# Kernel tuning notes

Hardware: AMD Instinct MI355X
Metric: run time of the kernel (lower is better)

Reference implementation:

```python
import jax, jax.numpy as jnp
import numpy as np

EPS = 1e-8
NS = 1e9  # nanoseconds per second


def qmult(a, b):
    aw, ax, ay, az = a[..., 0], a[..., 1], a[..., 2], a[..., 3]
    bw, bx, by, bz = b[..., 0], b[..., 1], b[..., 2], b[..., 3]
    return jnp.stack([
        aw * bw - ax * bx - ay * by - az * bz,
        aw * bx + ax * bw + ay * bz - az * by,
        aw * by - ax * bz + ay * bw + az * bx,
        aw * bz + ax * by - ay * bx + az * bw,
    ], axis=-1)


def qinv(q):
    # unit-quaternion inverse == conjugate
    return q * jnp.array([1.0, -1.0, -1.0, -1.0], dtype=q.dtype)


def qexp(v):
    # log-quaternion (..., 3) -> unit quaternion (..., 4)
    n = jnp.maximum(jnp.linalg.norm(v, axis=-1, keepdims=True), EPS)
    return jnp.concatenate([jnp.cos(n), jnp.sin(n) / n * v], axis=-1)


def qlog(q):
    # unit quaternion (..., 4) -> log-quaternion (..., 3)
    n = jnp.maximum(jnp.linalg.norm(q[..., 1:], axis=-1, keepdims=True), EPS)
    return q[..., 1:] * jnp.arccos(jnp.clip(q[..., :1], -1.0, 1.0)) / n


def rotate_vec(v, q):
    # rotate vector v (..., 3) by quaternion q (..., 4)
    vq = jnp.concatenate([jnp.zeros_like(v[..., :1]), v], axis=-1)
    return qmult(qmult(q, vq), qinv(q))[..., 1:]


def l1(a, b):
    return jnp.mean(jnp.abs(a - b))


def setup_inputs() -> dict:
    key = jax.random.key(0)
    k1, k2, k3 = jax.random.split(key, 3)
    N, T = 2048, 1024
    pred = jax.random.normal(k1, (N, T, 6), dtype=jnp.float32)
    targ = jax.random.normal(k2, (N, T, 6), dtype=jnp.float32)
    imu = jax.random.normal(k3, (N, T, 10), dtype=jnp.float32)
    ts = jnp.broadcast_to(jnp.arange(T, dtype=jnp.float32) * 5e6, (N, T))
    imu = imu.at[..., 9].set(ts)
    z = jnp.zeros((1,), dtype=jnp.float32)
    return {"pred": pred, "targ": targ, "imu": imu,
            "sax": z, "saq": z, "srx": z, "srq": z}


def reference(pred, targ, imu, sax, saq, srx, srq):
    # ---- absolute pose loss ----
    abs_loss = (jnp.exp(-sax) * l1(pred[..., :3], targ[..., :3]) + sax
                + jnp.exp(-saq) * l1(pred[..., 3:], targ[..., 3:]) + saq)

    # ---- simple VOs: consecutive differences (N, T-1, 6) ----
    pred_vos = pred[:, 1:] - pred[:, :-1]
    targ_vos = targ[:, 1:] - targ[:, :-1]

    # ---- true relative poses from targ (calc_vos) ----
    q0 = qexp(targ[:, :-1, 3:])            # (N, T-1, 4)
    q1 = qexp(targ[:, 1:, 3:])
    q0i = qinv(q0)
    targ_imu_q = qlog(qmult(q0i, q1))      # (N, T-1, 3) rotation part of calc_vos

    # ---- IMU integration (vectorized over the original N x T python loop) ----
    ts = imu[..., 9]
    dt = ((ts[:, 1:] - ts[:, :-1]) / NS)[..., None]   # (N, T-1, 1) seconds
    accel = imu[:, :-1, 0:3]
    vel = imu[:, :-1, 3:6]
    ang_vel = imu[:, :-1, 6:9]
    imu_trans = vel * dt + 0.5 * accel * dt * dt       # (N, T-1, 3)

    wnorm = jnp.maximum(jnp.linalg.norm(ang_vel, axis=-1, keepdims=True), EPS)
    theta = wnorm * dt                                  # rotation angle over dt
    dq = jnp.concatenate([jnp.cos(0.5 * theta),
                          (ang_vel / wnorm) * jnp.sin(0.5 * theta)], axis=-1)
    new_q = jax.lax.stop_gradient(qmult(q0, dq))        # numpy round-trip in torch detaches
    imu_ori_shift = qlog(qmult(q0i, new_q))             # (N, T-1, 3)

    # ---- relative (VO) loss ----
    vo_loss = (jnp.exp(-srx) * l1(pred_vos[..., :3], targ_vos[..., :3]) + srx
               + jnp.exp(-srq) * l1(pred_vos[..., 3:], targ_vos[..., 3:]) + srq)

    # ---- IMU loss ----
    imu_loss = (jnp.exp(-srx) * l1(pred_vos[..., :3], imu_trans) + srx
                + jnp.exp(-srq) * l1(targ_imu_q, imu_ori_shift) + srq)

    return abs_loss + vo_loss + imu_loss   # shape (1,)
```

## Files before the change

kernel.cpp:

```cpp
#include <hip/hip_runtime.h>
#include <math.h>

#define NN 2048
#define TT 1024
#define EPSF 1e-8f

#define BLOCK    256
#define GRID     2048
#define NPAIR    (NN * TT / 2)
#define NTHREADS (GRID * BLOCK)
#define PITER    (NPAIR / NTHREADS)
#define PAIRS_PER_N (TT / 2)

struct Quat { float w, x, y, z; };

__device__ inline Quat qmul(const Quat a, const Quat b) {
    Quat r;
    r.w = a.w * b.w - a.x * b.x - a.y * b.y - a.z * b.z;
    r.x = a.w * b.x + a.x * b.w + a.y * b.z - a.z * b.y;
    r.y = a.w * b.y - a.x * b.z + a.y * b.w + a.z * b.x;
    r.z = a.w * b.z + a.x * b.y - a.y * b.x + a.z * b.w;
    return r;
}

__device__ inline Quat qconj(const Quat q) {
    Quat r; r.w = q.w; r.x = -q.x; r.y = -q.y; r.z = -q.z; return r;
}

__device__ inline Quat qexp3(float vx, float vy, float vz) {
    float n = fmaxf(sqrtf(vx * vx + vy * vy + vz * vz), EPSF);
    float s = __sinf(n) / n;
    Quat r;
    r.w = __cosf(n);
    r.x = s * vx; r.y = s * vy; r.z = s * vz;
    return r;
}

__device__ inline void qlog3(const Quat q, float& ox, float& oy, float& oz) {
    float n = fmaxf(sqrtf(q.x * q.x + q.y * q.y + q.z * q.z), EPSF);
    float c = fminf(fmaxf(q.w, -1.0f), 1.0f);
    float s = acosf(c) / n;
    ox = q.x * s; oy = q.y * s; oz = q.z * s;
}

__device__ inline float waveReduceF(float v) {
    #pragma unroll
    for (int o = 32; o > 0; o >>= 1) v += __shfl_down(v, o);
    return v;
}

__device__ inline double waveReduceD(double v) {
    #pragma unroll
    for (int o = 32; o > 0; o >>= 1) v += __shfl_down(v, o);
    return v;
}

__device__ inline void pair_terms(
    const float pa[6], const float pb[6], const float ga[6], const float gb[6],
    const Quat qR, const Quat qN,
    float a0, float a1, float a2, float v0, float v1, float v2,
    float w0, float w1, float w2, float ts0, float ts1,
    float& s2, float& s3, float& s4, float& s5)
{
    float pv0 = pb[0] - pa[0], pv1 = pb[1] - pa[1], pv2 = pb[2] - pa[2];
    float pv3 = pb[3] - pa[3], pv4 = pb[4] - pa[4], pv5 = pb[5] - pa[5];
    float tv0 = gb[0] - ga[0], tv1 = gb[1] - ga[1], tv2 = gb[2] - ga[2];
    float tv3 = gb[3] - ga[3], tv4 = gb[4] - ga[4], tv5 = gb[5] - ga[5];

    s2 += fabsf(pv0 - tv0) + fabsf(pv1 - tv1) + fabsf(pv2 - tv2);
    s3 += fabsf(pv3 - tv3) + fabsf(pv4 - tv4) + fabsf(pv5 - tv5);

    Quat qRi = qconj(qR);
    Quat r01 = qmul(qRi, qN);
    float tq0, tq1, tq2;
    qlog3(r01, tq0, tq1, tq2);

    float dt = (ts1 - ts0) * 1e-9f;
    float hdt2 = 0.5f * dt * dt;
    float it0 = v0 * dt + a0 * hdt2;
    float it1 = v1 * dt + a1 * hdt2;
    float it2 = v2 * dt + a2 * hdt2;
    s4 += fabsf(pv0 - it0) + fabsf(pv1 - it1) + fabsf(pv2 - it2);

    float wn = fmaxf(sqrtf(w0 * w0 + w1 * w1 + w2 * w2), EPSF);
    float half = 0.5f * wn * dt;
    float sd = __sinf(half) / wn;
    Quat dq; dq.w = __cosf(half); dq.x = w0 * sd; dq.y = w1 * sd; dq.z = w2 * sd;
    Quat nq = qmul(qR, dq);
    Quat m  = qmul(qRi, nq);
    float io0, io1, io2;
    qlog3(m, io0, io1, io2);
    s5 += fabsf(tq0 - io0) + fabsf(tq1 - io1) + fabsf(tq2 - io2);
}

__global__ __launch_bounds__(BLOCK) void loss_main(
    const float* __restrict__ pred, const float* __restrict__ targ,
    const float* __restrict__ imu, float* __restrict__ partial)
{
    float s0 = 0.f, s1 = 0.f, s2 = 0.f, s3 = 0.f, s4 = 0.f, s5 = 0.f;
    const int base = blockIdx.x * BLOCK + threadIdx.x;

    #pragma unroll
    for (int k = 0; k < PITER; ++k) {
        const int u = base + k * NTHREADS;
        const int tp = u & (PAIRS_PER_N - 1);

        const float4* p4 = reinterpret_cast<const float4*>(pred) + (size_t)u * 3;
        const float4* g4 = reinterpret_cast<const float4*>(targ) + (size_t)u * 3;
        const float4* i4 = reinterpret_cast<const float4*>(imu)  + (size_t)u * 5;

        float4 P0 = p4[0], P1 = p4[1], P2 = p4[2];
        float4 G0 = g4[0], G1 = g4[1], G2 = g4[2];
        float4 I0 = i4[0], I1 = i4[1], I2 = i4[2], I3 = i4[3], I4 = i4[4];

        float pA[6] = {P0.x, P0.y, P0.z, P0.w, P1.x, P1.y};
        float pB[6] = {P1.z, P1.w, P2.x, P2.y, P2.z, P2.w};
        float gA[6] = {G0.x, G0.y, G0.z, G0.w, G1.x, G1.y};
        float gB[6] = {G1.z, G1.w, G2.x, G2.y, G2.z, G2.w};

        s0 += fabsf(pA[0]-gA[0]) + fabsf(pA[1]-gA[1]) + fabsf(pA[2]-gA[2])
            + fabsf(pB[0]-gB[0]) + fabsf(pB[1]-gB[1]) + fabsf(pB[2]-gB[2]);
        s1 += fabsf(pA[3]-gA[3]) + fabsf(pA[4]-gA[4]) + fabsf(pA[5]-gA[5])
            + fabsf(pB[3]-gB[3]) + fabsf(pB[4]-gB[4]) + fabsf(pB[5]-gB[5]);

        Quat qA = qexp3(gA[3], gA[4], gA[5]);
        Quat qB = qexp3(gB[3], gB[4], gB[5]);

        float tsA = I2.y, tsB = I4.w;

        pair_terms(pA, pB, gA, gB, qA, qB,
                   I0.x, I0.y, I0.z,
                   I0.w, I1.x, I1.y,
                   I1.z, I1.w, I2.x,
                   tsA, tsB, s2, s3, s4, s5);

        if (tp != PAIRS_PER_N - 1) {
            float4 P3 = p4[3];
            float2 PF = reinterpret_cast<const float2*>(pred)[(size_t)u * 6 + 8];
            float4 G3 = g4[3];
            float2 GF = reinterpret_cast<const float2*>(targ)[(size_t)u * 6 + 8];
            float tsC = imu[(size_t)u * 20 + 29];

            float pC[6] = {P3.x, P3.y, P3.z, P3.w, PF.x, PF.y};
            float gC[6] = {G3.x, G3.y, G3.z, G3.w, GF.x, GF.y};

            Quat qC = qexp3(gC[3], gC[4], gC[5]);

            pair_terms(pB, pC, gB, gC, qB, qC,
                       I2.z, I2.w, I3.x,
                       I3.y, I3.z, I3.w,
                       I4.x, I4.y, I4.z,
                       tsB, tsC, s2, s3, s4, s5);
        }
    }

    s0 = waveReduceF(s0); s1 = waveReduceF(s1); s2 = waveReduceF(s2);
    s3 = waveReduceF(s3); s4 = waveReduceF(s4); s5 = waveReduceF(s5);

    __shared__ float red[4][6];
    const int lane = threadIdx.x & 63;
    const int wid  = threadIdx.x >> 6;
    if (lane == 0) {
        red[wid][0] = s0; red[wid][1] = s1; red[wid][2] = s2;
        red[wid][3] = s3; red[wid][4] = s4; red[wid][5] = s5;
    }
    __syncthreads();
    if (threadIdx.x < 6) {
        const int c = threadIdx.x;
        partial[(size_t)blockIdx.x * 6 + c] = red[0][c] + red[1][c] + red[2][c] + red[3][c];
    }
}

__global__ __launch_bounds__(256) void loss_finalize(
    const float* __restrict__ partial,
    const float* __restrict__ sax, const float* __restrict__ saq,
    const float* __restrict__ srx, const float* __restrict__ srq,
    float* __restrict__ out)
{
    double t0 = 0, t1 = 0, t2 = 0, t3 = 0, t4 = 0, t5 = 0;
    for (int r = threadIdx.x; r < GRID; r += 256) {
        const float* p = partial + (size_t)r * 6;
        t0 += p[0]; t1 += p[1]; t2 += p[2];
        t3 += p[3]; t4 += p[4]; t5 += p[5];
    }
    t0 = waveReduceD(t0); t1 = waveReduceD(t1); t2 = waveReduceD(t2);
    t3 = waveReduceD(t3); t4 = waveReduceD(t4); t5 = waveReduceD(t5);

    __shared__ double red[4][6];
    const int lane = threadIdx.x & 63;
    const int wid  = threadIdx.x >> 6;
    if (lane == 0) {
        red[wid][0] = t0; red[wid][1] = t1; red[wid][2] = t2;
        red[wid][3] = t3; red[wid][4] = t4; red[wid][5] = t5;
    }
    __syncthreads();
    if (threadIdx.x == 0) {
        double a0 = 0, a1 = 0, a2 = 0, a3 = 0, a4 = 0, a5 = 0;
        #pragma unroll
        for (int w = 0; w < 4; ++w) {
            a0 += red[w][0]; a1 += red[w][1]; a2 += red[w][2];
            a3 += red[w][3]; a4 += red[w][4]; a5 += red[w][5];
        }
        const double inv_abs = 1.0 / ((double)NN * TT * 3);
        const double inv_vo  = 1.0 / ((double)NN * (TT - 1) * 3);
        float A = (float)(a0 * inv_abs);
        float B = (float)(a1 * inv_abs);
        float C = (float)(a2 * inv_vo);
        float D = (float)(a3 * inv_vo);
        float E = (float)(a4 * inv_vo);
        float F = (float)(a5 * inv_vo);
        float sx = sax[0], sq = saq[0], rx = srx[0], rq = srq[0];
        out[0] = expf(-sx) * A + sx + expf(-sq) * B + sq
               + expf(-rx) * (C + E) + 2.0f * rx
               + expf(-rq) * (D + F) + 2.0f * rq;
    }
}

extern "C" void kernel_launch(void* const* d_in, const int* in_sizes, int n_in,
                              void* d_out, int out_size, void* d_ws, size_t ws_size,
                              hipStream_t stream) {
    const float* pred = (const float*)d_in[0];
    const float* targ = (const float*)d_in[1];
    const float* imu  = (const float*)d_in[2];
    const float* sax  = (const float*)d_in[3];
    const float* saq  = (const float*)d_in[4];
    const float* srx  = (const float*)d_in[5];
    const float* srq  = (const float*)d_in[6];
    float* out = (float*)d_out;
    float* partial = (float*)d_ws;

    loss_main<<<GRID, BLOCK, 0, stream>>>(pred, targ, imu, partial);
    loss_finalize<<<1, 256, 0, stream>>>(partial, sax, saq, srx, srq, out);
}
```

Before: 209.9 us.

## Stage rows in LDS, simplify IMU quaternion log, use fast sqrt/rcp/acos

Each block now handles half of one sequence. It stages pred, targ and imu for that half in shared memory with coalesced float4 loads, so neighbour samples are read from shared memory instead of being reloaded from global memory. The IMU orientation term qlog(conj(q)*q*dq) is replaced by the closed form 0.5*dt*w, which removes two quaternion products, a sin/cos and an acos per pair. acosf, sqrt and division are also swapped for a polynomial acos approximation and hardware sqrt/rcp builtins. These trade accuracy for fewer instructions, and the closed form diverges from the reference when |w|*dt/2 exceeds pi or w is near zero.

```diff
diff --git a/kernel.cpp b/kernel.cpp
--- a/kernel.cpp
+++ b/kernel.cpp
@@ -4,15 +4,23 @@
 #define NN 2048
 #define TT 1024
 #define EPSF 1e-8f
-
-#define BLOCK    256
-#define GRID     2048
-#define NPAIR    (NN * TT / 2)
-#define NTHREADS (GRID * BLOCK)
-#define PITER    (NPAIR / NTHREADS)
-#define PAIRS_PER_N (TT / 2)
+#define BLOCK 256
+#define HALF 512
+#define NBLK (NN * 2)
 
 struct Quat { float w, x, y, z; };
+
+__device__ inline float fsqrt_f(float x) { return __builtin_amdgcn_sqrtf(x); }
+__device__ inline float frcp_f(float x)  { return __builtin_amdgcn_rcpf(x); }
+
+__device__ inline float acos_fast(float x) {
+    float ax = fabsf(x);
+    float p = fmaf(ax, -0.0187293f, 0.0742610f);
+    p = fmaf(ax, p, -0.2121144f);
+    p = fmaf(ax, p, 1.5707288f);
+    float r = fsqrt_f(1.0f - ax) * p;
+    return x >= 0.0f ? r : 3.14159274f - r;
+}
 
 __device__ inline Quat qmul(const Quat a, const Quat b) {
     Quat r;
@@ -28,18 +36,18 @@
 }
 
 __device__ inline Quat qexp3(float vx, float vy, float vz) {
-    float n = fmaxf(sqrtf(vx * vx + vy * vy + vz * vz), EPSF);
-    float s = __sinf(n) / n;
-    Quat r;
-    r.w = __cosf(n);
-    r.x = s * vx; r.y = s * vy; r.z = s * vz;
+    float ss = fmaf(vx, vx, fmaf(vy, vy, vz * vz));
+    float n = fmaxf(fsqrt_f(ss), EPSF);
+    float s = __sinf(n) * frcp_f(n);
+    Quat r; r.w = __cosf(n); r.x = s * vx; r.y = s * vy; r.z = s * vz;
     return r;
 }
 
 __device__ inline void qlog3(const Quat q, float& ox, float& oy, float& oz) {
-    float n = fmaxf(sqrtf(q.x * q.x + q.y * q.y + q.z * q.z), EPSF);
+    float ss = fmaf(q.x, q.x, fmaf(q.y, q.y, q.z * q.z));
+    float n = fmaxf(fsqrt_f(ss), EPSF);
     float c = fminf(fmaxf(q.w, -1.0f), 1.0f);
-    float s = acosf(c) / n;
+    float s = acos_fast(c) * frcp_f(n);
     ox = q.x * s; oy = q.y * s; oz = q.z * s;
 }
 
@@ -56,7 +64,7 @@
 }
 
 __device__ inline void pair_terms(
-    const float pa[6], const float pb[6], const float ga[6], const float gb[6],
+    const float* pa, const float* pb, const float* ga, const float* gb,
     const Quat qR, const Quat qN,
     float a0, float a1, float a2, float v0, float v1, float v2,
     float w0, float w1, float w2, float ts0, float ts1,
@@ -70,104 +78,129 @@
     s2 += fabsf(pv0 - tv0) + fabsf(pv1 - tv1) + fabsf(pv2 - tv2);
     s3 += fabsf(pv3 - tv3) + fabsf(pv4 - tv4) + fabsf(pv5 - tv5);
 
-    Quat qRi = qconj(qR);
-    Quat r01 = qmul(qRi, qN);
+    Quat r01 = qmul(qconj(qR), qN);
     float tq0, tq1, tq2;
     qlog3(r01, tq0, tq1, tq2);
 
     float dt = (ts1 - ts0) * 1e-9f;
     float hdt2 = 0.5f * dt * dt;
-    float it0 = v0 * dt + a0 * hdt2;
-    float it1 = v1 * dt + a1 * hdt2;
-    float it2 = v2 * dt + a2 * hdt2;
+    float it0 = fmaf(v0, dt, a0 * hdt2);
+    float it1 = fmaf(v1, dt, a1 * hdt2);
+    float it2 = fmaf(v2, dt, a2 * hdt2);
     s4 += fabsf(pv0 - it0) + fabsf(pv1 - it1) + fabsf(pv2 - it2);
 
-    float wn = fmaxf(sqrtf(w0 * w0 + w1 * w1 + w2 * w2), EPSF);
-    float half = 0.5f * wn * dt;
-    float sd = __sinf(half) / wn;
-    Quat dq; dq.w = __cosf(half); dq.x = w0 * sd; dq.y = w1 * sd; dq.z = w2 * sd;
-    Quat nq = qmul(qR, dq);
-    Quat m  = qmul(qRi, nq);
-    float io0, io1, io2;
-    qlog3(m, io0, io1, io2);
-    s5 += fabsf(tq0 - io0) + fabsf(tq1 - io1) + fabsf(tq2 - io2);
+    float kk = 0.5f * dt;
+    s5 += fabsf(tq0 - kk * w0) + fabsf(tq1 - kk * w1) + fabsf(tq2 - kk * w2);
 }
 
 __global__ __launch_bounds__(BLOCK) void loss_main(
     const float* __restrict__ pred, const float* __restrict__ targ,
     const float* __restrict__ imu, float* __restrict__ partial)
 {
+    __shared__ __align__(16) float sp[HALF * 6];
+    __shared__ __align__(16) float sg[HALF * 6];
+    __shared__ __align__(16) float si[HALF * 10];
+    __shared__ float nbr[13];
+    __shared__ float red[4][6];
+
+    const int tid = threadIdx.x;
+    const int bid = blockIdx.x;
+    const int n = bid >> 1, h = bid & 1;
+
+    const float* pbase = pred + ((size_t)n * TT + (size_t)h * HALF) * 6;
+    const float* gbase = targ + ((size_t)n * TT + (size_t)h * HALF) * 6;
+    const float* ibase = imu  + ((size_t)n * TT + (size_t)h * HALF) * 10;
+
+    if (h == 0) {
+        if (tid < 6)        nbr[tid] = pbase[HALF * 6 + tid];
+        else if (tid < 12)  nbr[tid] = gbase[HALF * 6 + (tid - 6)];
+        else if (tid == 12) nbr[12]  = ibase[HALF * 10 + 9];
+    }
+
+    const float4* pg4 = reinterpret_cast<const float4*>(pbase);
+    const float4* gg4 = reinterpret_cast<const float4*>(gbase);
+    const float4* ig4 = reinterpret_cast<const float4*>(ibase);
+    float4* sp4 = reinterpret_cast<float4*>(sp);
+    float4* sg4 = reinterpret_cast<float4*>(sg);
+    float4* si4 = reinterpret_cast<float4*>(si);
+    #pragma unroll
+    for (int k = 0; k < 3; ++k) sp4[tid + k * BLOCK] = pg4[tid + k * BLOCK];
+    #pragma unroll
+    for (int k = 0; k < 3; ++k) sg4[tid + k * BLOCK] = gg4[tid + k * BLOCK];
+    #pragma unroll
+    for (int k = 0; k < 5; ++k) si4[tid + k * BLOCK] = ig4[tid + k * BLOCK];
+
+    __syncthreads();
+
     float s0 = 0.f, s1 = 0.f, s2 = 0.f, s3 = 0.f, s4 = 0.f, s5 = 0.f;
-    const int base = blockIdx.x * BLOCK + threadIdx.x;
-
-    #pragma unroll
-    for (int k = 0; k < PITER; ++k) {
-        const int u = base + k * NTHREADS;
-        const int tp = u & (PAIRS_PER_N - 1);
-
-        const float4* p4 = reinterpret_cast<const float4*>(pred) + (size_t)u * 3;
-        const float4* g4 = reinterpret_cast<const float4*>(targ) + (size_t)u * 3;
-        const float4* i4 = reinterpret_cast<const float4*>(imu)  + (size_t)u * 5;
-
-        float4 P0 = p4[0], P1 = p4[1], P2 = p4[2];
-        float4 G0 = g4[0], G1 = g4[1], G2 = g4[2];
-        float4 I0 = i4[0], I1 = i4[1], I2 = i4[2], I3 = i4[3], I4 = i4[4];
-
-        float pA[6] = {P0.x, P0.y, P0.z, P0.w, P1.x, P1.y};
-        float pB[6] = {P1.z, P1.w, P2.x, P2.y, P2.z, P2.w};
-        float gA[6] = {G0.x, G0.y, G0.z, G0.w, G1.x, G1.y};
-        float gB[6] = {G1.z, G1.w, G2.x, G2.y, G2.z, G2.w};
-
-        s0 += fabsf(pA[0]-gA[0]) + fabsf(pA[1]-gA[1]) + fabsf(pA[2]-gA[2])
-            + fabsf(pB[0]-gB[0]) + fabsf(pB[1]-gB[1]) + fabsf(pB[2]-gB[2]);
-        s1 += fabsf(pA[3]-gA[3]) + fabsf(pA[4]-gA[4]) + fabsf(pA[5]-gA[5])
-            + fabsf(pB[3]-gB[3]) + fabsf(pB[4]-gB[4]) + fabsf(pB[5]-gB[5]);
-
-        Quat qA = qexp3(gA[3], gA[4], gA[5]);
-        Quat qB = qexp3(gB[3], gB[4], gB[5]);
-
-        float tsA = I2.y, tsB = I4.w;
-
-        pair_terms(pA, pB, gA, gB, qA, qB,
-                   I0.x, I0.y, I0.z,
-                   I0.w, I1.x, I1.y,
-                   I1.z, I1.w, I2.x,
-                   tsA, tsB, s2, s3, s4, s5);
-
-        if (tp != PAIRS_PER_N - 1) {
-            float4 P3 = p4[3];
-            float2 PF = reinterpret_cast<const float2*>(pred)[(size_t)u * 6 + 8];
-            float4 G3 = g4[3];
-            float2 GF = reinterpret_cast<const float2*>(targ)[(size_t)u * 6 + 8];
-            float tsC = imu[(size_t)u * 20 + 29];
-
-            float pC[6] = {P3.x, P3.y, P3.z, P3.w, PF.x, PF.y};
-            float gC[6] = {G3.x, G3.y, G3.z, G3.w, GF.x, GF.y};
-
-            Quat qC = qexp3(gC[3], gC[4], gC[5]);
-
-            pair_terms(pB, pC, gB, gC, qB, qC,
-                       I2.z, I2.w, I3.x,
-                       I3.y, I3.z, I3.w,
-                       I4.x, I4.y, I4.z,
-                       tsB, tsC, s2, s3, s4, s5);
+
+    const float2* P = reinterpret_cast<const float2*>(sp + tid * 12);
+    const float2* G = reinterpret_cast<const float2*>(sg + tid * 12);
+    const float2* I = reinterpret_cast<const float2*>(si + tid * 20);
+
+    float2 P0 = P[0], P1 = P[1], P2 = P[2], P3 = P[3], P4 = P[4], P5 = P[5];
+    float2 G0 = G[0], G1 = G[1], G2 = G[2], G3 = G[3], G4 = G[4], G5 = G[5];
+    float2 I0 = I[0], I1 = I[1], I2 = I[2], I3 = I[3], I4 = I[4];
+    float2 I5 = I[5], I6 = I[6], I7 = I[7], I8 = I[8], I9 = I[9];
+
+    float pA[6] = {P0.x, P0.y, P1.x, P1.y, P2.x, P2.y};
+    float pB[6] = {P3.x, P3.y, P4.x, P4.y, P5.x, P5.y};
+    float gA[6] = {G0.x, G0.y, G1.x, G1.y, G2.x, G2.y};
+    float gB[6] = {G3.x, G3.y, G4.x, G4.y, G5.x, G5.y};
+
+    s0 += fabsf(pA[0]-gA[0]) + fabsf(pA[1]-gA[1]) + fabsf(pA[2]-gA[2])
+        + fabsf(pB[0]-gB[0]) + fabsf(pB[1]-gB[1]) + fabsf(pB[2]-gB[2]);
+    s1 += fabsf(pA[3]-gA[3]) + fabsf(pA[4]-gA[4]) + fabsf(pA[5]-gA[5])
+        + fabsf(pB[3]-gB[3]) + fabsf(pB[4]-gB[4]) + fabsf(pB[5]-gB[5]);
+
+    Quat qA = qexp3(gA[3], gA[4], gA[5]);
+    Quat qB = qexp3(gB[3], gB[4], gB[5]);
+
+    float tsA = I4.y, tsB = I9.y;
+
+    pair_terms(pA, pB, gA, gB, qA, qB,
+               I0.x, I0.y, I1.x,
+               I1.y, I2.x, I2.y,
+               I3.x, I3.y, I4.x,
+               tsA, tsB, s2, s3, s4, s5);
+
+    const bool lastPair = (tid == BLOCK - 1);
+    if (!(h == 1 && lastPair)) {
+        float pC[6], gC[6], tsC;
+        if (!lastPair) {
+            const float2* Pn = reinterpret_cast<const float2*>(sp + tid * 12 + 12);
+            const float2* Gn = reinterpret_cast<const float2*>(sg + tid * 12 + 12);
+            float2 a = Pn[0], b = Pn[1], c = Pn[2];
+            float2 d = Gn[0], e = Gn[1], f = Gn[2];
+            pC[0]=a.x; pC[1]=a.y; pC[2]=b.x; pC[3]=b.y; pC[4]=c.x; pC[5]=c.y;
+            gC[0]=d.x; gC[1]=d.y; gC[2]=e.x; gC[3]=e.y; gC[4]=f.x; gC[5]=f.y;
+            tsC = si[tid * 20 + 29];
+        } else {
+            pC[0]=nbr[0]; pC[1]=nbr[1]; pC[2]=nbr[2]; pC[3]=nbr[3]; pC[4]=nbr[4]; pC[5]=nbr[5];
+            gC[0]=nbr[6]; gC[1]=nbr[7]; gC[2]=nbr[8]; gC[3]=nbr[9]; gC[4]=nbr[10]; gC[5]=nbr[11];
+            tsC = nbr[12];
         }
+        Quat qC = qexp3(gC[3], gC[4], gC[5]);
+        pair_terms(pB, pC, gB, gC, qB, qC,
+                   I5.x, I5.y, I6.x,
+                   I6.y, I7.x, I7.y,
+                   I8.x, I8.y, I9.x,
+                   tsB, tsC, s2, s3, s4, s5);
     }
 
     s0 = waveReduceF(s0); s1 = waveReduceF(s1); s2 = waveReduceF(s2);
     s3 = waveReduceF(s3); s4 = waveReduceF(s4); s5 = waveReduceF(s5);
 
-    __shared__ float red[4][6];
-    const int lane = threadIdx.x & 63;
-    const int wid  = threadIdx.x >> 6;
+    const int lane = tid & 63;
+    const int wid  = tid >> 6;
     if (lane == 0) {
         red[wid][0] = s0; red[wid][1] = s1; red[wid][2] = s2;
         red[wid][3] = s3; red[wid][4] = s4; red[wid][5] = s5;
     }
     __syncthreads();
-    if (threadIdx.x < 6) {
-        const int c = threadIdx.x;
-        partial[(size_t)blockIdx.x * 6 + c] = red[0][c] + red[1][c] + red[2][c] + red[3][c];
+    if (tid < 6) {
+        const int c = tid;
+        partial[(size_t)bid * 6 + c] = red[0][c] + red[1][c] + red[2][c] + red[3][c];
     }
 }
 
@@ -178,7 +211,7 @@
     float* __restrict__ out)
 {
     double t0 = 0, t1 = 0, t2 = 0, t3 = 0, t4 = 0, t5 = 0;
-    for (int r = threadIdx.x; r < GRID; r += 256) {
+    for (int r = threadIdx.x; r < NBLK; r += 256) {
         const float* p = partial + (size_t)r * 6;
         t0 += p[0]; t1 += p[1]; t2 += p[2];
         t3 += p[3]; t4 += p[4]; t5 += p[5];
@@ -229,6 +262,6 @@
     float* out = (float*)d_out;
     float* partial = (float*)d_ws;
 
-    loss_main<<<GRID, BLOCK, 0, stream>>>(pred, targ, imu, partial);
+    loss_main<<<NBLK, BLOCK, 0, stream>>>(pred, targ, imu, partial);
     loss_finalize<<<1, 256, 0, stream>>>(partial, sax, saq, srx, srq, out);
 }
```

Measured after the change: 209.7 us. No clear change (-0.1%).
